# Kernel optimization log

Hardware: AMD Instinct MI355X
Metric: run time of the kernel (lower is better)

The kernel has to match this reference:

```python
import jax, jax.numpy as jnp
import numpy as np

NUM_HEADS = 12
NUM_LANDMARKS = 64
DIM = 768


def _iterative_inv(mat, n_iter=6):
    # mat: [B, H, L, L]
    L = mat.shape[-1]
    I = jnp.eye(L, dtype=mat.dtype)
    K = mat
    # init: V = K^T / max_j(sum_i K_ij), scalar per (B, H)
    denom = jnp.max(jnp.sum(K, axis=-2), axis=-1)[:, :, None, None]
    V = (1.0 / denom) * jnp.swapaxes(K, -1, -2)
    for _ in range(n_iter):
        KV = jnp.matmul(K, V)
        V = jnp.matmul(0.25 * V, 13.0 * I - jnp.matmul(KV, 15.0 * I - jnp.matmul(KV, 7.0 * I - KV)))
    return V


def setup_inputs() -> dict:
    key = jax.random.key(0)
    k1, k2, k3, k4 = jax.random.split(key, 4)
    B, N, C = 4, 4096, DIM
    x = jax.random.normal(k1, (B, N, C), dtype=jnp.float32)
    w_qkv = jax.random.normal(k2, (3 * C, C), dtype=jnp.float32) * (C ** -0.5)
    w_proj = jax.random.normal(k3, (C, C), dtype=jnp.float32) * (C ** -0.5)
    b_proj = jax.random.normal(k4, (C,), dtype=jnp.float32) * 0.01
    return {"x": x, "w_qkv": w_qkv, "w_proj": w_proj, "b_proj": b_proj}


def reference(x, w_qkv, w_proj, b_proj):
    B, N, C = x.shape
    H, Lm = NUM_HEADS, NUM_LANDMARKS
    hd = C // H
    scale = hd ** 0.5
    # qkv: [3, B, H, N, hd]
    qkv = (x @ w_qkv.T).reshape(B, N, 3, H, hd).transpose(2, 0, 3, 1, 4)
    q, k, v = qkv[0], qkv[1], qkv[2]
    q = q / scale  # scaling happens BEFORE landmark pooling, as in source
    segs = N // Lm  # N % Lm == 0 path
    keys_landmarks = k.reshape(B, H, Lm, segs, hd).mean(axis=-2)      # [B,H,Lm,hd]
    queries_landmarks = q.reshape(B, H, Lm, segs, hd).mean(axis=-2)   # [B,H,Lm,hd]
    kernel_1 = jax.nn.softmax(jnp.einsum('bhnd,bhld->bhnl', q, keys_landmarks), axis=-1)            # [B,H,N,Lm]
    kernel_2 = jax.nn.softmax(jnp.einsum('bhmd,bhld->bhml', queries_landmarks, keys_landmarks), axis=-1)  # [B,H,Lm,Lm]
    kernel_3 = jax.nn.softmax(jnp.einsum('bhld,bhnd->bhln', queries_landmarks, k), axis=-1)         # [B,H,Lm,N]
    out = jnp.matmul(jnp.matmul(kernel_1, _iterative_inv(kernel_2)), jnp.matmul(kernel_3, v))       # [B,H,N,hd]
    out = out.transpose(0, 2, 1, 3).reshape(B, N, C)
    return out @ w_proj.T + b_proj
```

## Files before the change

kernel.cpp:

```cpp
#include <hip/hip_runtime.h>
#include <hip/hip_bf16.h>

#define DI __device__ __forceinline__

typedef __attribute__((ext_vector_type(8))) short bh8;
typedef __attribute__((ext_vector_type(8))) unsigned short us8;
typedef __attribute__((ext_vector_type(4))) float f4ev;

static constexpr int Bn = 4;
static constexpr int Nn = 4096;
static constexpr int Cn = 768;
static constexpr int Hn = 12;
static constexpr int Dn = 64;
static constexpr int Ln = 64;
static constexpr int TOKS = Bn * Nn;
static constexpr int BHn = Bn * Hn;

static constexpr size_t SZ_XB  = (size_t)TOKS * Cn * 2;
static constexpr size_t SZ_QKV = (size_t)BHn * Nn * Dn * 2;
static constexpr size_t OFF_XB   = 0;
static constexpr size_t OFF_QB   = OFF_XB + SZ_XB;
static constexpr size_t OFF_KB   = OFF_QB + SZ_QKV;
static constexpr size_t OFF_VB   = OFF_KB + SZ_QKV;
static constexpr size_t OFF_WQB  = OFF_VB + SZ_QKV;
static constexpr size_t OFF_WPB  = OFF_WQB + (size_t)3 * Cn * Cn * 2;
static constexpr size_t OFF_XM   = OFF_WPB + (size_t)Cn * Cn * 2;
static constexpr size_t OFF_QL   = OFF_XM + (size_t)Bn * Ln * Cn * 4;
static constexpr size_t OFF_KL   = OFF_QL + (size_t)Bn * Ln * Cn * 4;
static constexpr size_t OFF_VINV = OFF_KL + (size_t)Bn * Ln * Cn * 4;
static constexpr size_t OFF_CP   = OFF_VINV + (size_t)BHn * 64 * 64 * 4;
static constexpr size_t OFF_W2   = OFF_CP + (size_t)BHn * 32 * 64 * 2 * 4;

DI unsigned short f2bf(float f) {
  __hip_bfloat16 h = __float2bfloat16(f);
  return *reinterpret_cast<unsigned short*>(&h);
}
DI float bf2f(unsigned short u) {
  union { unsigned int i; float f; } c; c.i = ((unsigned)u) << 16; return c.f;
}

DI void gload_lds16(const void* g, void* l) {
  __builtin_amdgcn_global_load_lds((const __attribute__((address_space(1))) void*)g,
                                   (__attribute__((address_space(3))) void*)l, 16, 0, 0);
}

__global__ void cast_k(const float* __restrict__ s, unsigned short* __restrict__ d, int n4) {
  int i = blockIdx.x * blockDim.x + threadIdx.x;
  int st = gridDim.x * blockDim.x;
  const float4* s4 = (const float4*)s;
  ushort4* d4 = (ushort4*)d;
  for (; i < n4; i += st) {
    float4 v = s4[i];
    ushort4 o; o.x = f2bf(v.x); o.y = f2bf(v.y); o.z = f2bf(v.z); o.w = f2bf(v.w);
    d4[i] = o;
  }
}

__global__ void castmean_k(const float* __restrict__ x, unsigned short* __restrict__ xb,
                           float* __restrict__ xm) {
  int bl = blockIdx.x, cz = blockIdx.y;
  int c = cz * 384 + threadIdx.x * 2;
  const float* xp = x + (size_t)bl * 64 * Cn + c;
  unsigned short* xbp = xb + (size_t)bl * 64 * Cn + c;
  float s0 = 0.f, s1 = 0.f;
  #pragma unroll 8
  for (int r = 0; r < 64; ++r) {
    float2 v = *(const float2*)(xp + (size_t)r * Cn);
    ushort2 o; o.x = f2bf(v.x); o.y = f2bf(v.y);
    *(ushort2*)(xbp + (size_t)r * Cn) = o;
    s0 += v.x; s1 += v.y;
  }
  xm[(size_t)bl * Cn + c]     = s0 * 0.015625f;
  xm[(size_t)bl * Cn + c + 1] = s1 * 0.015625f;
}

__launch_bounds__(256)
__global__ void landgemm_k(const float* __restrict__ xm, const float* __restrict__ wqkv,
                           float* __restrict__ part) {
  __shared__ float XT[64][65];
  __shared__ float WT[64][65];
  int b = blockIdx.x, ct = blockIdx.y, kc = blockIdx.z;
  int t = threadIdx.x;
  int tr = t >> 4, tc = t & 15;
  int r0 = tr * 4, j0 = tc * 4;
  const float* xb_ = xm + (size_t)b * Ln * Cn + kc * 64;
  const float* wb_ = wqkv + (size_t)ct * 64 * Cn + kc * 64;
  #pragma unroll
  for (int i = t; i < 1024; i += 256) {
    int r = i >> 4, c4 = (i & 15) * 4;
    float4 xv = *(const float4*)(xb_ + (size_t)r * Cn + c4);
    XT[c4 + 0][r] = xv.x; XT[c4 + 1][r] = xv.y; XT[c4 + 2][r] = xv.z; XT[c4 + 3][r] = xv.w;
    float4 wv = *(const float4*)(wb_ + (size_t)r * Cn + c4);
    WT[c4 + 0][r] = wv.x; WT[c4 + 1][r] = wv.y; WT[c4 + 2][r] = wv.z; WT[c4 + 3][r] = wv.w;
  }
  __syncthreads();
  float acc[4][4];
  #pragma unroll
  for (int i = 0; i < 4; ++i)
    #pragma unroll
    for (int j = 0; j < 4; ++j) acc[i][j] = 0.f;
  for (int cc = 0; cc < 64; ++cc) {
    float4 a4 = *(const float4*)&XT[cc][r0];
    float4 b4 = *(const float4*)&WT[cc][j0];
    acc[0][0] += a4.x * b4.x; acc[0][1] += a4.x * b4.y; acc[0][2] += a4.x * b4.z; acc[0][3] += a4.x * b4.w;
    acc[1][0] += a4.y * b4.x; acc[1][1] += a4.y * b4.y; acc[1][2] += a4.y * b4.z; acc[1][3] += a4.y * b4.w;
    acc[2][0] += a4.z * b4.x; acc[2][1] += a4.z * b4.y; acc[2][2] += a4.z * b4.z; acc[2][3] += a4.z * b4.w;
    acc[3][0] += a4.w * b4.x; acc[3][1] += a4.w * b4.y; acc[3][2] += a4.w * b4.z; acc[3][3] += a4.w * b4.w;
  }
  float* op = part + ((size_t)kc * 256 + b * Ln) * 1536 + (size_t)ct * 64;
  #pragma unroll
  for (int i = 0; i < 4; ++i)
    *(float4*)(op + (size_t)(r0 + i) * 1536 + j0) = make_float4(acc[i][0], acc[i][1], acc[i][2], acc[i][3]);
}

__global__ void landred_k(const float* __restrict__ part, float* __restrict__ ql,
                          float* __restrict__ kl) {
  int i4 = blockIdx.x * 256 + threadIdx.x;
  const float4* p4 = (const float4*)part;
  float4 s = p4[i4];
  #pragma unroll
  for (int kc = 1; kc < 12; ++kc) {
    float4 v = p4[(size_t)kc * 98304 + i4];
    s.x += v.x; s.y += v.y; s.z += v.z; s.w += v.w;
  }
  int row = i4 / 384, c = (i4 % 384) * 4;
  if (c < 768) {
    s.x *= 0.125f; s.y *= 0.125f; s.z *= 0.125f; s.w *= 0.125f;
    *(float4*)(ql + (size_t)row * Cn + c) = s;
  } else {
    *(float4*)(kl + (size_t)row * Cn + (c - 768)) = s;
  }
}

__launch_bounds__(256)
__global__ void k2inv_k(const float* __restrict__ ql, const float* __restrict__ kl,
                        float* __restrict__ vinv) {
  __shared__ float B0[64][68], B1[64][68], B2[64][68], B3[64][68],
                   B4[64][68], B5[64][68], B6[64][68], B7[64][68];
  __shared__ float dinv_s;
  float (*Qt)[68] = B0, (*Kt)[68] = B1;
  float (*KV)[68] = B0, (*KVt)[68] = B1;
  float (*K2)[68] = B2, (*K2t)[68] = B3;
  float (*Vv)[68] = B4, (*Vt)[68] = B5;
  float (*T1)[68] = B6, (*Uu)[68] = B7;

  int bh = blockIdx.x, b = bh / Hn, h = bh % Hn;
  int t = threadIdx.x;
  int tr = t >> 4, tc = t & 15;
  int r0 = tr * 4, j0 = tc * 4;

  {
    const float* qbase = ql + (size_t)(b * Ln) * Cn + h * Dn;
    const float* kbase = kl + (size_t)(b * Ln) * Cn + h * Dn;
    #pragma unroll
    for (int it = 0; it < 4; ++it) {
      int idx = it * 256 + t;
      int l = idx >> 4, d0 = (idx & 15) * 4;
      float4 qv = *(const float4*)(qbase + (size_t)l * Cn + d0);
      float4 kv = *(const float4*)(kbase + (size_t)l * Cn + d0);
      Qt[d0 + 0][l] = qv.x; Qt[d0 + 1][l] = qv.y; Qt[d0 + 2][l] = qv.z; Qt[d0 + 3][l] = qv.w;
      Kt[d0 + 0][l] = kv.x; Kt[d0 + 1][l] = kv.y; Kt[d0 + 2][l] = kv.z; Kt[d0 + 3][l] = kv.w;
    }
  }
  __syncthreads();

  float acc[4][4];
  #define MM64(LT, RR)                                                     \
    {                                                                      \
      _Pragma("unroll")                                                    \
      for (int i_ = 0; i_ < 4; ++i_)                                       \
        _Pragma("unroll")                                                  \
        for (int j_ = 0; j_ < 4; ++j_) acc[i_][j_] = 0.f;                  \
      for (int c_ = 0; c_ < 64; c_ += 4) {                                 \
        _Pragma("unroll")                                                  \
        for (int cc_ = 0; cc_ < 4; ++cc_) {                                \
          float4 a4 = *(const float4*)&LT[c_ + cc_][r0];                   \
          float4 b4 = *(const float4*)&RR[c_ + cc_][j0];                   \
          acc[0][0] += a4.x * b4.x; acc[0][1] += a4.x * b4.y;              \
          acc[0][2] += a4.x * b4.z; acc[0][3] += a4.x * b4.w;              \
          acc[1][0] += a4.y * b4.x; acc[1][1] += a4.y * b4.y;              \
          acc[1][2] += a4.y * b4.z; acc[1][3] += a4.y * b4.w;              \
          acc[2][0] += a4.z * b4.x; acc[2][1] += a4.z * b4.y;              \
          acc[2][2] += a4.z * b4.z; acc[2][3] += a4.z * b4.w;              \
          acc[3][0] += a4.w * b4.x; acc[3][1] += a4.w * b4.y;              \
          acc[3][2] += a4.w * b4.z; acc[3][3] += a4.w * b4.w;              \
        }                                                                  \
      }                                                                    \
    }

  MM64(Qt, Kt);
  #pragma unroll
  for (int i = 0; i < 4; ++i)
    *(float4*)&K2[r0 + i][j0] = make_float4(acc[i][0], acc[i][1], acc[i][2], acc[i][3]);
  __syncthreads();

  if (t < 64) {
    float m = -1e30f;
    #pragma unroll
    for (int c4 = 0; c4 < 16; ++c4) {
      float4 v = *(const float4*)&K2[t][c4 * 4];
      m = fmaxf(m, fmaxf(fmaxf(v.x, v.y), fmaxf(v.z, v.w)));
    }
    float s = 0.f;
    #pragma unroll
    for (int c4 = 0; c4 < 16; ++c4) {
      float4 v = *(const float4*)&K2[t][c4 * 4];
      v.x = __expf(v.x - m); v.y = __expf(v.y - m);
      v.z = __expf(v.z - m); v.w = __expf(v.w - m);
      s += v.x + v.y + v.z + v.w;
      *(float4*)&K2[t][c4 * 4] = v;
    }
    float inv = 1.f / s;
    #pragma unroll
    for (int c4 = 0; c4 < 16; ++c4) {
      float4 v = *(const float4*)&K2[t][c4 * 4];
      v.x *= inv; v.y *= inv; v.z *= inv; v.w *= inv;
      *(float4*)&K2[t][c4 * 4] = v;
      K2t[c4 * 4 + 0][t] = v.x; K2t[c4 * 4 + 1][t] = v.y;
      K2t[c4 * 4 + 2][t] = v.z; K2t[c4 * 4 + 3][t] = v.w;
    }
  }
  __syncthreads();
  if (t < 64) {
    float cs = 0.f;
    #pragma unroll
    for (int c4 = 0; c4 < 16; ++c4) {
      float4 v = *(const float4*)&K2t[t][c4 * 4];
      cs += v.x + v.y + v.z + v.w;
    }
    #pragma unroll
    for (int off = 1; off < 64; off <<= 1) cs = fmaxf(cs, __shfl_xor(cs, off));
    if (t == 0) dinv_s = 1.f / cs;
  }
  __syncthreads();
  float dinv = dinv_s;
  #pragma unroll
  for (int jj = 0; jj < 4; ++jj) {
    float4 k4 = *(const float4*)&K2[j0 + jj][r0];
    k4.x *= dinv; k4.y *= dinv; k4.z *= dinv; k4.w *= dinv;
    *(float4*)&Vt[j0 + jj][r0] = k4;
    Vv[r0 + 0][j0 + jj] = k4.x; Vv[r0 + 1][j0 + jj] = k4.y;
    Vv[r0 + 2][j0 + jj] = k4.z; Vv[r0 + 3][j0 + jj] = k4.w;
  }
  __syncthreads();

  float nv[4][4];
  for (int itn = 0; itn < 6; ++itn) {
    MM64(K2t, Vv);
    #pragma unroll
    for (int i = 0; i < 4; ++i)
      *(float4*)&KV[r0 + i][j0] = make_float4(acc[i][0], acc[i][1], acc[i][2], acc[i][3]);
    #pragma unroll
    for (int jj = 0; jj < 4; ++jj)
      *(float4*)&KVt[j0 + jj][r0] = make_float4(acc[0][jj], acc[1][jj], acc[2][jj], acc[3][jj]);
    __syncthreads();
    MM64(KVt, KV);
    #pragma unroll
    for (int i = 0; i < 4; ++i) {
      float4 kv4 = *(const float4*)&KV[r0 + i][j0];
      *(float4*)&T1[r0 + i][j0] = make_float4(7.f * kv4.x - acc[i][0], 7.f * kv4.y - acc[i][1],
                                              7.f * kv4.z - acc[i][2], 7.f * kv4.w - acc[i][3]);
    }
    __syncthreads();
    MM64(KVt, T1);
    #pragma unroll
    for (int i = 0; i < 4; ++i) {
      float4 kv4 = *(const float4*)&KV[r0 + i][j0];
      *(float4*)&Uu[r0 + i][j0] = make_float4(15.f * kv4.x - acc[i][0], 15.f * kv4.y - acc[i][1],
                                              15.f * kv4.z - acc[i][2], 15.f * kv4.w - acc[i][3]);
    }
    __syncthreads();
    MM64(Vt, Uu);
    #pragma unroll
    for (int i = 0; i < 4; ++i) {
      float4 v4 = *(const float4*)&Vv[r0 + i][j0];
      nv[i][0] = 0.25f * (13.f * v4.x - acc[i][0]);
      nv[i][1] = 0.25f * (13.f * v4.y - acc[i][1]);
      nv[i][2] = 0.25f * (13.f * v4.z - acc[i][2]);
      nv[i][3] = 0.25f * (13.f * v4.w - acc[i][3]);
    }
    __syncthreads();
    #pragma unroll
    for (int i = 0; i < 4; ++i)
      *(float4*)&Vv[r0 + i][j0] = make_float4(nv[i][0], nv[i][1], nv[i][2], nv[i][3]);
    #pragma unroll
    for (int jj = 0; jj < 4; ++jj)
      *(float4*)&Vt[j0 + jj][r0] = make_float4(nv[0][jj], nv[1][jj], nv[2][jj], nv[3][jj]);
    __syncthreads();
  }
  float* op = vinv + (size_t)bh * 4096;
  #pragma unroll
  for (int i = 0; i < 4; ++i)
    *(float4*)(op + (size_t)(r0 + i) * 64 + j0) = make_float4(nv[i][0], nv[i][1], nv[i][2], nv[i][3]);
  #undef MM64
}

__launch_bounds__(256)
__global__ void gemm_qkv_k(const __hip_bfloat16* __restrict__ A, const __hip_bfloat16* __restrict__ W,
                           __hip_bfloat16* __restrict__ qb, __hip_bfloat16* __restrict__ kb,
                           __hip_bfloat16* __restrict__ vb) {
  __shared__ unsigned short As[128][64], Bs[128][64];
  int t = threadIdx.x, lane = t & 63, w = t >> 6;
  int wr = w >> 1, wc = w & 1;
  int m0 = blockIdx.x * 128, n0 = blockIdx.y * 128;
  int srow = w * 8 + (lane >> 3);
  int scol = ((lane & 7) ^ ((lane >> 3) & 7)) * 8;
  f4ev acc[4][4];
  f4ev zz = {0.f, 0.f, 0.f, 0.f};
  #pragma unroll
  for (int m = 0; m < 4; ++m)
    #pragma unroll
    for (int n = 0; n < 4; ++n) acc[m][n] = zz;
  const __hip_bfloat16* ga = A + (size_t)(m0 + srow) * Cn + scol;
  const __hip_bfloat16* gb = W + (size_t)(n0 + srow) * Cn + scol;
  for (int k0 = 0; k0 < Cn; k0 += 64) {
    #pragma unroll
    for (int c = 0; c < 4; ++c) {
      gload_lds16(ga + (size_t)(c * 32) * Cn + k0, &As[c * 32 + w * 8][0]);
      gload_lds16(gb + (size_t)(c * 32) * Cn + k0, &Bs[c * 32 + w * 8][0]);
    }
    __syncthreads();
    #pragma unroll
    for (int ks = 0; ks < 2; ++ks) {
      int pc = ((ks * 4 + (lane >> 4)) ^ (lane & 7)) * 8;
      bh8 af[4], bf_[4];
      #pragma unroll
      for (int m = 0; m < 4; ++m)
        af[m] = *(const bh8*)&As[wr * 64 + m * 16 + (lane & 15)][pc];
      #pragma unroll
      for (int n = 0; n < 4; ++n)
        bf_[n] = *(const bh8*)&Bs[wc * 64 + n * 16 + (lane & 15)][pc];
      #pragma unroll
      for (int m = 0; m < 4; ++m)
        #pragma unroll
        for (int n = 0; n < 4; ++n)
          acc[m][n] = __builtin_amdgcn_mfma_f32_16x16x32_bf16(af[m], bf_[n], acc[m][n], 0, 0, 0);
    }
    __syncthreads();
  }
  int which = (n0 >= 1536) ? 2 : (n0 >= 768 ? 1 : 0);
  __hip_bfloat16* dst = which == 0 ? qb : (which == 1 ? kb : vb);
  float sc = which == 0 ? 0.125f : 1.f;
  #pragma unroll
  for (int m = 0; m < 4; ++m) {
    int rbase = m0 + wr * 64 + m * 16 + ((lane >> 4) << 2);
    #pragma unroll
    for (int n = 0; n < 4; ++n) {
      int c = n0 + wc * 64 + n * 16 + (lane & 15);
      int rem = c - which * 768;
      int h = rem >> 6, dd = rem & 63;
      #pragma unroll
      for (int jj = 0; jj < 4; ++jj) {
        int r = rbase + jj;
        int b = r >> 12, ntok = r & 4095;
        dst[(((size_t)(b * Hn + h) * Nn + ntok) << 6) + dd] = __float2bfloat16(acc[m][n][jj] * sc);
      }
    }
  }
}

__launch_bounds__(256)
__global__ void k3vflash_k(const float* __restrict__ ql, const __hip_bfloat16* __restrict__ kb,
                           const __hip_bfloat16* __restrict__ vb,
                           float* __restrict__ ocp, float* __restrict__ stat) {
  __shared__ unsigned short Ks[128][72];
  __shared__ unsigned short VT[64][136];
  auto Pl = (unsigned short (*)[136]) & Ks[0][0];
  int ch = blockIdx.x, bh = blockIdx.y;
  int b = bh / Hn, h = bh % Hn;
  int t = threadIdx.x, lane = t & 63, w = t >> 6;

  {
    int row = t >> 1, half = (t & 1) * 32;
    const us8* krow = (const us8*)((const unsigned short*)kb + ((size_t)bh * Nn + (size_t)ch * 128 + row) * Dn + half);
    const us8* vrow = (const us8*)((const unsigned short*)vb + ((size_t)bh * Nn + (size_t)ch * 128 + row) * Dn + half);
    us8 kv0 = krow[0], kv1 = krow[1], kv2 = krow[2], kv3 = krow[3];
    us8 vv0 = vrow[0], vv1 = vrow[1], vv2 = vrow[2], vv3 = vrow[3];
    *(us8*)&Ks[row][half + 0]  = kv0;
    *(us8*)&Ks[row][half + 8]  = kv1;
    *(us8*)&Ks[row][half + 16] = kv2;
    *(us8*)&Ks[row][half + 24] = kv3;
    #pragma unroll
    for (int e = 0; e < 8; ++e) {
      VT[half + e][row]      = vv0[e];
      VT[half + 8 + e][row]  = vv1[e];
      VT[half + 16 + e][row] = vv2[e];
      VT[half + 24 + e][row] = vv3[e];
    }
  }
  bh8 aq[2];
  {
    const float* qrow = ql + ((size_t)(b * Ln + w * 16 + (lane & 15))) * Cn + h * Dn + (lane >> 4) * 8;
    #pragma unroll
    for (int ks = 0; ks < 2; ++ks) {
      float4 f0 = *(const float4*)(qrow + ks * 32);
      float4 f1 = *(const float4*)(qrow + ks * 32 + 4);
      bh8 v;
      v[0] = (short)f2bf(f0.x); v[1] = (short)f2bf(f0.y); v[2] = (short)f2bf(f0.z); v[3] = (short)f2bf(f0.w);
      v[4] = (short)f2bf(f1.x); v[5] = (short)f2bf(f1.y); v[6] = (short)f2bf(f1.z); v[7] = (short)f2bf(f1.w);
      aq[ks] = v;
    }
  }
  __syncthreads();
  f4ev sacc[8];
  f4ev zz = {0.f, 0.f, 0.f, 0.f};
  #pragma unroll
  for (int nt = 0; nt < 8; ++nt) sacc[nt] = zz;
  #pragma unroll
  for (int ks = 0; ks < 2; ++ks)
    #pragma unroll
    for (int nt = 0; nt < 8; ++nt) {
      bh8 bk = *(const bh8*)&Ks[nt * 16 + (lane & 15)][ks * 32 + (lane >> 4) * 8];
      sacc[nt] = __builtin_amdgcn_mfma_f32_16x16x32_bf16(aq[ks], bk, sacc[nt], 0, 0, 0);
    }
  float M[4];
  #pragma unroll
  for (int j = 0; j < 4; ++j) {
    float m = sacc[0][j];
    #pragma unroll
    for (int nt = 1; nt < 8; ++nt) m = fmaxf(m, sacc[nt][j]);
    m = fmaxf(m, __shfl_xor(m, 1));
    m = fmaxf(m, __shfl_xor(m, 2));
    m = fmaxf(m, __shfl_xor(m, 4));
    m = fmaxf(m, __shfl_xor(m, 8));
    M[j] = m;
  }
  __syncthreads();
  float Ssum[4] = {0.f, 0.f, 0.f, 0.f};
  #pragma unroll
  for (int nt = 0; nt < 8; ++nt)
    #pragma unroll
    for (int j = 0; j < 4; ++j) {
      float pf = __expf(sacc[nt][j] - M[j]);
      Ssum[j] += pf;
      Pl[w * 16 + (lane >> 4) * 4 + j][nt * 16 + (lane & 15)] = f2bf(pf);
    }
  #pragma unroll
  for (int j = 0; j < 4; ++j) {
    float s = Ssum[j];
    s += __shfl_xor(s, 1);
    s += __shfl_xor(s, 2);
    s += __shfl_xor(s, 4);
    s += __shfl_xor(s, 8);
    Ssum[j] = s;
  }
  if ((lane & 15) == 0) {
    #pragma unroll
    for (int j = 0; j < 4; ++j) {
      int l2 = w * 16 + (lane >> 4) * 4 + j;
      float* sp = stat + (((size_t)bh * 32 + ch) * 64 + l2) * 2;
      sp[0] = M[j]; sp[1] = Ssum[j];
    }
  }
  __syncthreads();
  f4ev oacc[4];
  #pragma unroll
  for (int nt = 0; nt < 4; ++nt) oacc[nt] = zz;
  #pragma unroll
  for (int ks = 0; ks < 4; ++ks) {
    bh8 ap = *(const bh8*)&Pl[w * 16 + (lane & 15)][ks * 32 + (lane >> 4) * 8];
    #pragma unroll
    for (int nt = 0; nt < 4; ++nt) {
      bh8 bv = *(const bh8*)&VT[nt * 16 + (lane & 15)][ks * 32 + (lane >> 4) * 8];
      oacc[nt] = __builtin_amdgcn_mfma_f32_16x16x32_bf16(ap, bv, oacc[nt], 0, 0, 0);
    }
  }
  float* ob = ocp + (((size_t)bh * 32 + ch) * 64) * 64;
  #pragma unroll
  for (int nt = 0; nt < 4; ++nt)
    #pragma unroll
    for (int j = 0; j < 4; ++j) {
      int l2 = w * 16 + ((lane >> 4) << 2) + j;
      ob[l2 * 64 + nt * 16 + (lane & 15)] = oacc[nt][j];
    }
}

__global__ void w2f_k(const float* __restrict__ ocp, const float* __restrict__ stat,
                      const float* __restrict__ vinv, float* __restrict__ w2) {
  __shared__ float kv[64][72], vi[64][72];
  __shared__ float wch[32][64];
  __shared__ float invS[64];
  int bh = blockIdx.x, t = threadIdx.x, j = t & 63, ig = t >> 6;
  if (t < 64) {
    const float* sp = stat + (size_t)bh * 32 * 128;
    float M = -1e30f;
    #pragma unroll
    for (int c = 0; c < 32; ++c) M = fmaxf(M, sp[c * 128 + t * 2]);
    float S = 0.f;
    #pragma unroll
    for (int c = 0; c < 32; ++c) {
      float wcb = __expf(sp[c * 128 + t * 2] - M);
      wch[c][t] = wcb;
      S += wcb * sp[c * 128 + t * 2 + 1];
    }
    invS[t] = 1.f / S;
  }
  for (int i = t; i < 4096; i += 256) vi[i >> 6][i & 63] = vinv[(size_t)bh * 4096 + i];
  __syncthreads();
  float acc[16];
  #pragma unroll
  for (int i = 0; i < 16; ++i) acc[i] = 0.f;
  const float* op = ocp + (size_t)bh * 32 * 4096;
  for (int c = 0; c < 32; ++c) {
    #pragma unroll
    for (int jj = 0; jj < 4; ++jj) {
      int i4 = t * 4 + jj * 1024;
      float4 v = *(const float4*)(op + (size_t)c * 4096 + i4);
      float wcb = wch[c][i4 >> 6];
      acc[jj * 4 + 0] += v.x * wcb;
      acc[jj * 4 + 1] += v.y * wcb;
      acc[jj * 4 + 2] += v.z * wcb;
      acc[jj * 4 + 3] += v.w * wcb;
    }
  }
  #pragma unroll
  for (int jj = 0; jj < 4; ++jj) {
    int i4 = t * 4 + jj * 1024;
    float is = invS[i4 >> 6];
    kv[i4 >> 6][(i4 & 63) + 0] = acc[jj * 4 + 0] * is;
    kv[i4 >> 6][(i4 & 63) + 1] = acc[jj * 4 + 1] * is;
    kv[i4 >> 6][(i4 & 63) + 2] = acc[jj * 4 + 2] * is;
    kv[i4 >> 6][(i4 & 63) + 3] = acc[jj * 4 + 3] * is;
  }
  __syncthreads();
  float a[16];
  #pragma unroll
  for (int li = 0; li < 16; ++li) a[li] = 0.f;
  for (int c2 = 0; c2 < 64; ++c2) {
    float vv = kv[c2][j];
    #pragma unroll
    for (int li = 0; li < 16; ++li) a[li] += vi[ig * 16 + li][c2] * vv;
  }
  #pragma unroll
  for (int li = 0; li < 16; ++li) w2[(size_t)bh * 4096 + (ig * 16 + li) * 64 + j] = a[li];
}

__launch_bounds__(256)
__global__ void k1app_k(const __hip_bfloat16* __restrict__ qb, const float* __restrict__ kl,
                        const float* __restrict__ w2, __hip_bfloat16* __restrict__ oh) {
  __shared__ unsigned short SM[128 * 72 + 64 * 72 * 2];
  auto Klhi = (unsigned short (*)[72])(SM);
  auto Kllo = (unsigned short (*)[72])(SM + 64 * 72);
  auto Pl   = (unsigned short (*)[72])(SM);
  auto Whi  = (unsigned short (*)[72])(SM + 128 * 72);
  auto Wlo  = (unsigned short (*)[72])(SM + 128 * 72 + 64 * 72);

  int ch = blockIdx.x, bh = blockIdx.y;
  int b = bh / Hn, h = bh % Hn;
  int t = threadIdx.x, lane = t & 63, w = t >> 6;

  {
    const float* klb = kl + (size_t)(b * Ln) * Cn + h * Dn;
    const float* w2b = w2 + (size_t)bh * 4096;
    #pragma unroll
    for (int it = 0; it < 4; ++it) {
      int idx = it * 256 + t;
      int l = idx >> 4, d0 = (idx & 15) * 4;
      float4 kv = *(const float4*)(klb + (size_t)l * Cn + d0);
      ushort4 hi4; ushort4 lo4;
      hi4.x = f2bf(kv.x); lo4.x = f2bf(kv.x - bf2f(hi4.x));
      hi4.y = f2bf(kv.y); lo4.y = f2bf(kv.y - bf2f(hi4.y));
      hi4.z = f2bf(kv.z); lo4.z = f2bf(kv.z - bf2f(hi4.z));
      hi4.w = f2bf(kv.w); lo4.w = f2bf(kv.w - bf2f(hi4.w));
      *(ushort4*)&Klhi[l][d0] = hi4;
      *(ushort4*)&Kllo[l][d0] = lo4;
      float4 wv = *(const float4*)(w2b + (size_t)l * 64 + d0);
      unsigned short h0 = f2bf(wv.x), h1 = f2bf(wv.y), h2 = f2bf(wv.z), h3 = f2bf(wv.w);
      Whi[d0 + 0][l] = h0; Wlo[d0 + 0][l] = f2bf(wv.x - bf2f(h0));
      Whi[d0 + 1][l] = h1; Wlo[d0 + 1][l] = f2bf(wv.y - bf2f(h1));
      Whi[d0 + 2][l] = h2; Wlo[d0 + 2][l] = f2bf(wv.z - bf2f(h2));
      Whi[d0 + 3][l] = h3; Wlo[d0 + 3][l] = f2bf(wv.w - bf2f(h3));
    }
  }
  bh8 aq[2][2];
  {
    const unsigned short* qbase = (const unsigned short*)qb + ((size_t)bh * Nn + (size_t)ch * 128) * Dn;
    #pragma unroll
    for (int m = 0; m < 2; ++m)
      #pragma unroll
      for (int ks = 0; ks < 2; ++ks)
        aq[m][ks] = *(const bh8*)(qbase + (size_t)(w * 32 + m * 16 + (lane & 15)) * Dn + ks * 32 + (lane >> 4) * 8);
  }
  __syncthreads();
  f4ev sacc[2][4];
  f4ev zz = {0.f, 0.f, 0.f, 0.f};
  #pragma unroll
  for (int m = 0; m < 2; ++m)
    #pragma unroll
    for (int nt = 0; nt < 4; ++nt) sacc[m][nt] = zz;
  #pragma unroll
  for (int ks = 0; ks < 2; ++ks)
    #pragma unroll
    for (int nt = 0; nt < 4; ++nt) {
      bh8 bhi = *(const bh8*)&Klhi[nt * 16 + (lane & 15)][ks * 32 + (lane >> 4) * 8];
      bh8 blo = *(const bh8*)&Kllo[nt * 16 + (lane & 15)][ks * 32 + (lane >> 4) * 8];
      #pragma unroll
      for (int m = 0; m < 2; ++m) {
        sacc[m][nt] = __builtin_amdgcn_mfma_f32_16x16x32_bf16(aq[m][ks], bhi, sacc[m][nt], 0, 0, 0);
        sacc[m][nt] = __builtin_amdgcn_mfma_f32_16x16x32_bf16(aq[m][ks], blo, sacc[m][nt], 0, 0, 0);
      }
    }
  float Pn[2][4][4];
  #pragma unroll
  for (int m = 0; m < 2; ++m)
    #pragma unroll
    for (int j = 0; j < 4; ++j) {
      float mx = sacc[m][0][j];
      #pragma unroll
      for (int nt = 1; nt < 4; ++nt) mx = fmaxf(mx, sacc[m][nt][j]);
      mx = fmaxf(mx, __shfl_xor(mx, 1));
      mx = fmaxf(mx, __shfl_xor(mx, 2));
      mx = fmaxf(mx, __shfl_xor(mx, 4));
      mx = fmaxf(mx, __shfl_xor(mx, 8));
      float sum = 0.f;
      #pragma unroll
      for (int nt = 0; nt < 4; ++nt) {
        float e = __expf(sacc[m][nt][j] - mx);
        Pn[m][nt][j] = e;
        sum += e;
      }
      sum += __shfl_xor(sum, 1);
      sum += __shfl_xor(sum, 2);
      sum += __shfl_xor(sum, 4);
      sum += __shfl_xor(sum, 8);
      float inv = 1.f / sum;
      #pragma unroll
      for (int nt = 0; nt < 4; ++nt) Pn[m][nt][j] *= inv;
    }
  __syncthreads();
  #pragma unroll
  for (int m = 0; m < 2; ++m)
    #pragma unroll
    for (int nt = 0; nt < 4; ++nt)
      #pragma unroll
      for (int j = 0; j < 4; ++j)
        Pl[w * 32 + m * 16 + (lane >> 4) * 4 + j][nt * 16 + (lane & 15)] = f2bf(Pn[m][nt][j]);
  __syncthreads();
  f4ev oacc[2][4];
  #pragma unroll
  for (int m = 0; m < 2; ++m)
    #pragma unroll
    for (int nt = 0; nt < 4; ++nt) oacc[m][nt] = zz;
  #pragma unroll
  for (int ks = 0; ks < 2; ++ks) {
    bh8 ap[2];
    #pragma unroll
    for (int m = 0; m < 2; ++m)
      ap[m] = *(const bh8*)&Pl[w * 32 + m * 16 + (lane & 15)][ks * 32 + (lane >> 4) * 8];
    #pragma unroll
    for (int nt = 0; nt < 4; ++nt) {
      bh8 bhi = *(const bh8*)&Whi[nt * 16 + (lane & 15)][ks * 32 + (lane >> 4) * 8];
      bh8 blo = *(const bh8*)&Wlo[nt * 16 + (lane & 15)][ks * 32 + (lane >> 4) * 8];
      #pragma unroll
      for (int m = 0; m < 2; ++m) {
        oacc[m][nt] = __builtin_amdgcn_mfma_f32_16x16x32_bf16(ap[m], bhi, oacc[m][nt], 0, 0, 0);
        oacc[m][nt] = __builtin_amdgcn_mfma_f32_16x16x32_bf16(ap[m], blo, oacc[m][nt], 0, 0, 0);
      }
    }
  }
  unsigned short* ohb = (unsigned short*)oh;
  #pragma unroll
  for (int m = 0; m < 2; ++m)
    #pragma unroll
    for (int nt = 0; nt < 4; ++nt)
      #pragma unroll
      for (int j = 0; j < 4; ++j) {
        int tok = ch * 128 + w * 32 + m * 16 + (lane >> 4) * 4 + j;
        int dd = nt * 16 + (lane & 15);
        ohb[((size_t)(b * Nn + tok)) * Cn + h * Dn + dd] = f2bf(oacc[m][nt][j]);
      }
}

__launch_bounds__(256)
__global__ void gemm_proj_k(const __hip_bfloat16* __restrict__ A, const __hip_bfloat16* __restrict__ W,
                            const float* __restrict__ bias, float* __restrict__ out) {
  __shared__ unsigned short As[128][64], Bs[128][64];
  int t = threadIdx.x, lane = t & 63, w = t >> 6;
  int wr = w >> 1, wc = w & 1;
  int m0 = blockIdx.x * 128, n0 = blockIdx.y * 128;
  int srow = w * 8 + (lane >> 3);
  int scol = ((lane & 7) ^ ((lane >> 3) & 7)) * 8;
  f4ev acc[4][4];
  f4ev zz = {0.f, 0.f, 0.f, 0.f};
  #pragma unroll
  for (int m = 0; m < 4; ++m)
    #pragma unroll
    for (int n = 0; n < 4; ++n) acc[m][n] = zz;
  const __hip_bfloat16* ga = A + (size_t)(m0 + srow) * Cn + scol;
  const __hip_bfloat16* gb = W + (size_t)(n0 + srow) * Cn + scol;
  for (int k0 = 0; k0 < Cn; k0 += 64) {
    #pragma unroll
    for (int c = 0; c < 4; ++c) {
      gload_lds16(ga + (size_t)(c * 32) * Cn + k0, &As[c * 32 + w * 8][0]);
      gload_lds16(gb + (size_t)(c * 32) * Cn + k0, &Bs[c * 32 + w * 8][0]);
    }
    __syncthreads();
    #pragma unroll
    for (int ks = 0; ks < 2; ++ks) {
      int pc = ((ks * 4 + (lane >> 4)) ^ (lane & 7)) * 8;
      bh8 af[4], bf_[4];
      #pragma unroll
      for (int m = 0; m < 4; ++m)
        af[m] = *(const bh8*)&As[wr * 64 + m * 16 + (lane & 15)][pc];
      #pragma unroll
      for (int n = 0; n < 4; ++n)
        bf_[n] = *(const bh8*)&Bs[wc * 64 + n * 16 + (lane & 15)][pc];
      #pragma unroll
      for (int m = 0; m < 4; ++m)
        #pragma unroll
        for (int n = 0; n < 4; ++n)
          acc[m][n] = __builtin_amdgcn_mfma_f32_16x16x32_bf16(af[m], bf_[n], acc[m][n], 0, 0, 0);
    }
    __syncthreads();
  }
  #pragma unroll
  for (int m = 0; m < 4; ++m) {
    int rbase = m0 + wr * 64 + m * 16 + ((lane >> 4) << 2);
    #pragma unroll
    for (int n = 0; n < 4; ++n) {
      int c = n0 + wc * 64 + n * 16 + (lane & 15);
      float bv = bias[c];
      #pragma unroll
      for (int jj = 0; jj < 4; ++jj)
        out[(size_t)(rbase + jj) * Cn + c] = acc[m][n][jj] + bv;
    }
  }
}

extern "C" void kernel_launch(void* const* d_in, const int* in_sizes, int n_in,
                              void* d_out, int out_size, void* d_ws, size_t ws_size,
                              hipStream_t stream) {
  const float* x     = (const float*)d_in[0];
  const float* wqkv  = (const float*)d_in[1];
  const float* wproj = (const float*)d_in[2];
  const float* bproj = (const float*)d_in[3];
  float* out = (float*)d_out;
  char* ws = (char*)d_ws;

  auto xb   = (__hip_bfloat16*)(ws + OFF_XB);
  auto qb   = (__hip_bfloat16*)(ws + OFF_QB);
  auto kb   = (__hip_bfloat16*)(ws + OFF_KB);
  auto vb   = (__hip_bfloat16*)(ws + OFF_VB);
  auto wqb  = (__hip_bfloat16*)(ws + OFF_WQB);
  auto wpb  = (__hip_bfloat16*)(ws + OFF_WPB);
  auto ocp  = (float*)(ws + OFF_XB);
  auto oh   = (__hip_bfloat16*)(ws + OFF_XB);
  auto part = (float*)(ws + OFF_QB);
  auto xm   = (float*)(ws + OFF_XM);
  auto ql   = (float*)(ws + OFF_QL);
  auto kl   = (float*)(ws + OFF_KL);
  auto vinv = (float*)(ws + OFF_VINV);
  auto cp   = (float*)(ws + OFF_CP);
  auto w2   = (float*)(ws + OFF_W2);

  castmean_k<<<dim3(256, 2), 192, 0, stream>>>(x, (unsigned short*)xb, xm);
  cast_k<<<1024, 256, 0, stream>>>(wqkv, (unsigned short*)wqb, 3 * Cn * Cn / 4);
  cast_k<<<512, 256, 0, stream>>>(wproj, (unsigned short*)wpb, Cn * Cn / 4);
  landgemm_k<<<dim3(4, 24, 12), 256, 0, stream>>>(xm, wqkv, part);
  landred_k<<<384, 256, 0, stream>>>(part, ql, kl);
  k2inv_k<<<48, 256, 0, stream>>>(ql, kl, vinv);
  gemm_qkv_k<<<dim3(128, 18), 256, 0, stream>>>(xb, wqb, qb, kb, vb);
  k3vflash_k<<<dim3(32, 48), 256, 0, stream>>>(ql, kb, vb, ocp, cp);
  w2f_k<<<48, 256, 0, stream>>>(ocp, cp, vinv, w2);
  k1app_k<<<dim3(32, 48), 256, 0, stream>>>(qb, kl, w2, oh);
  gemm_proj_k<<<dim3(128, 6), 256, 0, stream>>>(oh, wpb, bproj, out);
}
```

Before: 263.5 us.

## Remap GEMM workgroups for XCD locality and halve proj K-tile

Both the QKV and projection GEMMs switch to a 1D grid with a block-id remap. The remap groups consecutive tiles onto the same XCD (orig&7 selects the XCD), so blocks sharing A rows also share L2. The projection GEMM also shrinks its LDS K-tile from 64 to 32 and uses a new swizzle, cutting shared memory per block so more blocks can be resident. The cost is twice as many barrier-separated iterations in the projection loop, with less MFMA work per sync.

```diff
diff --git a/kernel.cpp b/kernel.cpp
--- a/kernel.cpp
+++ b/kernel.cpp
@@ -300,9 +300,12 @@
                            __hip_bfloat16* __restrict__ qb, __hip_bfloat16* __restrict__ kb,
                            __hip_bfloat16* __restrict__ vb) {
   __shared__ unsigned short As[128][64], Bs[128][64];
+  int orig = blockIdx.x;
+  int wg = (orig & 7) * 288 + (orig >> 3);
+  int mt = wg / 18, ntile = wg % 18;
+  int m0 = mt * 128, n0 = ntile * 128;
   int t = threadIdx.x, lane = t & 63, w = t >> 6;
   int wr = w >> 1, wc = w & 1;
-  int m0 = blockIdx.x * 128, n0 = blockIdx.y * 128;
   int srow = w * 8 + (lane >> 3);
   int scol = ((lane & 7) ^ ((lane >> 3) & 7)) * 8;
   f4ev acc[4][4];
@@ -674,43 +677,42 @@
 __launch_bounds__(256)
 __global__ void gemm_proj_k(const __hip_bfloat16* __restrict__ A, const __hip_bfloat16* __restrict__ W,
                             const float* __restrict__ bias, float* __restrict__ out) {
-  __shared__ unsigned short As[128][64], Bs[128][64];
+  __shared__ unsigned short As[128][32], Bs[128][32];
+  int orig = blockIdx.x;
+  int wg = (orig & 7) * 96 + (orig >> 3);
+  int mt = wg / 6, ntile = wg % 6;
+  int m0 = mt * 128, n0 = ntile * 128;
   int t = threadIdx.x, lane = t & 63, w = t >> 6;
   int wr = w >> 1, wc = w & 1;
-  int m0 = blockIdx.x * 128, n0 = blockIdx.y * 128;
-  int srow = w * 8 + (lane >> 3);
-  int scol = ((lane & 7) ^ ((lane >> 3) & 7)) * 8;
+  int srow = lane >> 2;
+  int scol = (((lane & 3) ^ ((lane >> 3) & 3))) * 8;
+  int rcol = (((lane >> 4) ^ ((lane >> 1) & 3))) * 8;
   f4ev acc[4][4];
   f4ev zz = {0.f, 0.f, 0.f, 0.f};
   #pragma unroll
   for (int m = 0; m < 4; ++m)
     #pragma unroll
     for (int n = 0; n < 4; ++n) acc[m][n] = zz;
-  const __hip_bfloat16* ga = A + (size_t)(m0 + srow) * Cn + scol;
-  const __hip_bfloat16* gb = W + (size_t)(n0 + srow) * Cn + scol;
-  for (int k0 = 0; k0 < Cn; k0 += 64) {
-    #pragma unroll
-    for (int c = 0; c < 4; ++c) {
-      gload_lds16(ga + (size_t)(c * 32) * Cn + k0, &As[c * 32 + w * 8][0]);
-      gload_lds16(gb + (size_t)(c * 32) * Cn + k0, &Bs[c * 32 + w * 8][0]);
-    }
-    __syncthreads();
-    #pragma unroll
-    for (int ks = 0; ks < 2; ++ks) {
-      int pc = ((ks * 4 + (lane >> 4)) ^ (lane & 7)) * 8;
-      bh8 af[4], bf_[4];
-      #pragma unroll
-      for (int m = 0; m < 4; ++m)
-        af[m] = *(const bh8*)&As[wr * 64 + m * 16 + (lane & 15)][pc];
+  const __hip_bfloat16* ga = A + (size_t)(m0 + w * 16 + srow) * Cn + scol;
+  const __hip_bfloat16* gb = W + (size_t)(n0 + w * 16 + srow) * Cn + scol;
+  for (int k0 = 0; k0 < Cn; k0 += 32) {
+    gload_lds16(ga + k0,                   &As[w * 16][0]);
+    gload_lds16(ga + (size_t)64 * Cn + k0, &As[64 + w * 16][0]);
+    gload_lds16(gb + k0,                   &Bs[w * 16][0]);
+    gload_lds16(gb + (size_t)64 * Cn + k0, &Bs[64 + w * 16][0]);
+    __syncthreads();
+    bh8 af[4], bf_[4];
+    #pragma unroll
+    for (int m = 0; m < 4; ++m)
+      af[m] = *(const bh8*)&As[wr * 64 + m * 16 + (lane & 15)][rcol];
+    #pragma unroll
+    for (int n = 0; n < 4; ++n)
+      bf_[n] = *(const bh8*)&Bs[wc * 64 + n * 16 + (lane & 15)][rcol];
+    #pragma unroll
+    for (int m = 0; m < 4; ++m)
       #pragma unroll
       for (int n = 0; n < 4; ++n)
-        bf_[n] = *(const bh8*)&Bs[wc * 64 + n * 16 + (lane & 15)][pc];
-      #pragma unroll
-      for (int m = 0; m < 4; ++m)
-        #pragma unroll
-        for (int n = 0; n < 4; ++n)
-          acc[m][n] = __builtin_amdgcn_mfma_f32_16x16x32_bf16(af[m], bf_[n], acc[m][n], 0, 0, 0);
-    }
+        acc[m][n] = __builtin_amdgcn_mfma_f32_16x16x32_bf16(af[m], bf_[n], acc[m][n], 0, 0, 0);
     __syncthreads();
   }
   #pragma unroll
@@ -759,9 +761,9 @@
   landgemm_k<<<dim3(4, 24, 12), 256, 0, stream>>>(xm, wqkv, part);
   landred_k<<<384, 256, 0, stream>>>(part, ql, kl);
   k2inv_k<<<48, 256, 0, stream>>>(ql, kl, vinv);
-  gemm_qkv_k<<<dim3(128, 18), 256, 0, stream>>>(xb, wqb, qb, kb, vb);
+  gemm_qkv_k<<<2304, 256, 0, stream>>>(xb, wqb, qb, kb, vb);
   k3vflash_k<<<dim3(32, 48), 256, 0, stream>>>(ql, kb, vb, ocp, cp);
   w2f_k<<<48, 256, 0, stream>>>(ocp, cp, vinv, w2);
   k1app_k<<<dim3(32, 48), 256, 0, stream>>>(qb, kl, w2, oh);
-  gemm_proj_k<<<dim3(128, 6), 256, 0, stream>>>(oh, wpb, bproj, out);
-}
+  gemm_proj_k<<<768, 256, 0, stream>>>(oh, wpb, bproj, out);
+}
```

Measured after the change: 259.6 us. No clear change (-1.5%).
